# Optimization experiments

Hardware: AMD Instinct MI355X
Metric: run time of the kernel (lower is better)

The kernel has to match this reference:

```python
import jax, jax.numpy as jnp
import numpy as np

N, D = 1024, 512
BS, N_TEXT, N_VIDEO = 64, 16, 16
BETA = 1.0
N_ITERS = 50


def setup_inputs() -> dict:
    key = jax.random.key(0)
    k1, k2 = jax.random.split(key)
    return {
        "t_prob": jax.random.normal(k1, (N, D), dtype=jnp.float32),
        "v_prob": jax.random.normal(k2, (N, D), dtype=jnp.float32),
        "n": N,
        "bs": BS,
        "n_text": N_TEXT,
        "n_video": N_VIDEO,
    }


def _l2norm(x):
    # matches F.normalize(x, p=2, dim=1) (eps irrelevant for randn inputs)
    return x / jnp.linalg.norm(x, axis=1, keepdims=True)


def reference(t_prob, v_prob, n, bs, n_text, n_video):
    dt = t_prob.dtype
    x = _l2norm(t_prob)
    y = _l2norm(v_prob)
    C = 1.0 - x @ y.T                      # [n, n] cosine distance
    A = jnp.exp(-C / BETA)

    sigma0 = jnp.ones((n, 1), dtype=dt) / n
    T0 = jnp.ones((n, n), dtype=dt)

    def step(carry, _):
        T, sigma = carry
        Q = A * T                          # [n, n]
        delta = 1.0 / (n * (Q @ sigma))    # [n, 1]
        sigma_new = 1.0 / (n * (Q.T @ delta))  # [n, 1]
        # diag(delta) @ Q @ diag(sigma) == row/col rescale
        T_new = delta * Q * sigma_new.T
        return (T_new, sigma_new), None

    (T, _), _ = jax.lax.scan(step, (T0, sigma0), None, length=N_ITERS)

    distance_matrix = C.T @ T              # [n, n]
    distance_matrix = distance_matrix.reshape(bs, n_text, bs, n_video).mean(axis=(1, 3))
    dis_loss = jnp.trace(distance_matrix)
    return distance_matrix, dis_loss
```

## Files before the change

kernel.cpp:

```cpp
#include <hip/hip_runtime.h>
#include <math.h>


#define NWG 32
#define TPB 1024
#define NIT 50
#define NREP 4

typedef unsigned long long ull;

constexpr int CL_OFF   = 0;
constexpr int CVEC_OFF = 1024 * 1024;
constexpr int CNT_OFF  = CVEC_OFF + 3 * NREP * 1024;

__global__ __launch_bounds__(256) void k_gemm(const float* __restrict__ X,
                                              const float* __restrict__ Y,
                                              float* __restrict__ ws) {
    __shared__ float As[32][68];
    __shared__ float Bs[32][68];
    __shared__ float nX[64], nY[64];
    float* Cl = ws + CL_OFF;

    int tid = threadIdx.x;
    int tx = tid & 15, ty = tid >> 4;
    int bx = blockIdx.x, by = blockIdx.y;
    int lr0 = tid >> 3;
    int kq  = (tid & 7) * 4;

    float acc[4][4] = {};
    float sx0 = 0.f, sx1 = 0.f, sy0 = 0.f, sy1 = 0.f;
    for (int k0 = 0; k0 < 512; k0 += 32) {
        float4 xa = *(const float4*)(X + (size_t)(by * 64 + lr0) * 512 + k0 + kq);
        float4 xb = *(const float4*)(X + (size_t)(by * 64 + lr0 + 32) * 512 + k0 + kq);
        float4 ya = *(const float4*)(Y + (size_t)(bx * 64 + lr0) * 512 + k0 + kq);
        float4 yb = *(const float4*)(Y + (size_t)(bx * 64 + lr0 + 32) * 512 + k0 + kq);
        sx0 += xa.x * xa.x + xa.y * xa.y + xa.z * xa.z + xa.w * xa.w;
        sx1 += xb.x * xb.x + xb.y * xb.y + xb.z * xb.z + xb.w * xb.w;
        sy0 += ya.x * ya.x + ya.y * ya.y + ya.z * ya.z + ya.w * ya.w;
        sy1 += yb.x * yb.x + yb.y * yb.y + yb.z * yb.z + yb.w * yb.w;
        As[kq + 0][lr0] = xa.x; As[kq + 1][lr0] = xa.y;
        As[kq + 2][lr0] = xa.z; As[kq + 3][lr0] = xa.w;
        As[kq + 0][lr0 + 32] = xb.x; As[kq + 1][lr0 + 32] = xb.y;
        As[kq + 2][lr0 + 32] = xb.z; As[kq + 3][lr0 + 32] = xb.w;
        Bs[kq + 0][lr0] = ya.x; Bs[kq + 1][lr0] = ya.y;
        Bs[kq + 2][lr0] = ya.z; Bs[kq + 3][lr0] = ya.w;
        Bs[kq + 0][lr0 + 32] = yb.x; Bs[kq + 1][lr0 + 32] = yb.y;
        Bs[kq + 2][lr0 + 32] = yb.z; Bs[kq + 3][lr0 + 32] = yb.w;
        __syncthreads();
#pragma unroll
        for (int kk = 0; kk < 32; ++kk) {
            float4 a4 = *(const float4*)&As[kk][4 * ty];
            float4 b4 = *(const float4*)&Bs[kk][4 * tx];
            float av[4] = {a4.x, a4.y, a4.z, a4.w};
            float bv[4] = {b4.x, b4.y, b4.z, b4.w};
#pragma unroll
            for (int r = 0; r < 4; ++r)
#pragma unroll
                for (int q = 0; q < 4; ++q) acc[r][q] += av[r] * bv[q];
        }
        __syncthreads();
    }
#pragma unroll
    for (int m = 1; m < 8; m <<= 1) {
        sx0 += __shfl_xor(sx0, m, 64);
        sx1 += __shfl_xor(sx1, m, 64);
        sy0 += __shfl_xor(sy0, m, 64);
        sy1 += __shfl_xor(sy1, m, 64);
    }
    if ((tid & 7) == 0) {
        nX[lr0] = sx0; nX[lr0 + 32] = sx1;
        nY[lr0] = sy0; nY[lr0 + 32] = sy1;
    }
    __syncthreads();

    int i0 = by * 64 + 4 * ty, j0 = bx * 64 + 4 * tx;
    float vy[4];
#pragma unroll
    for (int q = 0; q < 4; ++q) vy[q] = 1.0f / sqrtf(nY[4 * tx + q]);
#pragma unroll
    for (int r = 0; r < 4; ++r) {
        float vx = 1.0f / sqrtf(nX[4 * ty + r]);
        float4 o;
        o.x = acc[r][0] * vx * vy[0] - 1.0f;
        o.y = acc[r][1] * vx * vy[1] - 1.0f;
        o.z = acc[r][2] * vx * vy[2] - 1.0f;
        o.w = acc[r][3] * vx * vy[3] - 1.0f;
        *(float4*)(Cl + (size_t)(i0 + r) * 1024 + j0) = o;
    }
}

__global__ __launch_bounds__(1024, 4) void k_ipot(float* __restrict__ ws,
                                                  float* __restrict__ out) {
    __shared__ float sL[1024];
    __shared__ float aL[32];
    __shared__ float buf[16 * 1024];
    __shared__ float twv[16];

    const int g = blockIdx.x, tid = threadIdx.x;
    const int rs = tid >> 6, lane = tid & 63;
    float* Cl   = ws + CL_OFF;
    float* cvec = ws + CVEC_OFF;
    unsigned* grp = (unsigned*)(ws + CNT_OFF);

    float C[2][16], E[2][16];
#pragma unroll
    for (int i = 0; i < 2; ++i) {
        const float* src = Cl + (size_t)(g * 32 + rs * 2 + i) * 1024 + lane * 16;
#pragma unroll
        for (int q = 0; q < 4; ++q) {
            float4 c = *(const float4*)(src + 4 * q);
            C[i][4 * q + 0] = c.x; C[i][4 * q + 1] = c.y;
            C[i][4 * q + 2] = c.z; C[i][4 * q + 3] = c.w;
        }
    }
#pragma unroll
    for (int i = 0; i < 2; ++i)
#pragma unroll
        for (int u = 0; u < 16; ++u) E[i][u] = __expf(C[i][u]);

    float bv = 1.0f;

    for (int t = 0; t < NIT; ++t) {
        if (t == 0) {
            sL[tid] = 1.0f / 1024.0f;
        } else {
            if (tid == 0) {
                unsigned tgt = (unsigned)t * 8u;
                long gd = 0;
                while (__hip_atomic_load(&grp[0], __ATOMIC_RELAXED, __HIP_MEMORY_SCOPE_AGENT) < tgt ||
                       __hip_atomic_load(&grp[1], __ATOMIC_RELAXED, __HIP_MEMORY_SCOPE_AGENT) < tgt ||
                       __hip_atomic_load(&grp[2], __ATOMIC_RELAXED, __HIP_MEMORY_SCOPE_AGENT) < tgt ||
                       __hip_atomic_load(&grp[3], __ATOMIC_RELAXED, __HIP_MEMORY_SCOPE_AGENT) < tgt) {
                    __builtin_amdgcn_s_sleep(1);
                    if (++gd > 2000000) break;
                }
            }
            __syncthreads();
            const float* rb = cvec + ((t + 2) % 3) * (NREP * 1024) + tid;
            float r0 = __hip_atomic_load(rb + 0 * 1024, __ATOMIC_RELAXED, __HIP_MEMORY_SCOPE_AGENT);
            float r1 = __hip_atomic_load(rb + 1 * 1024, __ATOMIC_RELAXED, __HIP_MEMORY_SCOPE_AGENT);
            float r2 = __hip_atomic_load(rb + 2 * 1024, __ATOMIC_RELAXED, __HIP_MEMORY_SCOPE_AGENT);
            float r3 = __hip_atomic_load(rb + 3 * 1024, __ATOMIC_RELAXED, __HIP_MEMORY_SCOPE_AGENT);
            if (t >= 2 && tid < 64) {
                ull* zb = (ull*)(cvec + ((t + 1) % 3) * (NREP * 1024)) + g * 64 + tid;
                __hip_atomic_store(zb, 0ull, __ATOMIC_RELAXED, __HIP_MEMORY_SCOPE_AGENT);
            }
            float c = r0 + r1 + r2 + r3;
            float b = 1.0f / c;
            sL[tid] = b * b / bv * (1.0f / 1024.0f);
            bv = b;
        }
        __syncthreads();

        float sv[16];
#pragma unroll
        for (int q = 0; q < 4; ++q) {
            float4 s4 = *(const float4*)&sL[lane * 16 + 4 * q];
            sv[4 * q + 0] = s4.x; sv[4 * q + 1] = s4.y;
            sv[4 * q + 2] = s4.z; sv[4 * q + 3] = s4.w;
        }
        float rp[2];
#pragma unroll
        for (int i = 0; i < 2; ++i) {
            float a = 0.0f;
#pragma unroll
            for (int u = 0; u < 16; ++u) a += E[i][u] * sv[u];
            rp[i] = a;
        }
#pragma unroll
        for (int m = 1; m < 64; m <<= 1) {
            rp[0] += __shfl_xor(rp[0], m, 64);
            rp[1] += __shfl_xor(rp[1], m, 64);
        }
        if (lane == 0) {
            aL[rs * 2 + 0] = 1.0f / (1024.0f * rp[0]);
            aL[rs * 2 + 1] = 1.0f / (1024.0f * rp[1]);
        }
        __syncthreads();

        float av0 = aL[rs * 2 + 0], av1 = aL[rs * 2 + 1];
#pragma unroll
        for (int q = 0; q < 4; ++q) {
            float4 o;
            o.x = E[0][4*q+0] * av0 + E[1][4*q+0] * av1;
            o.y = E[0][4*q+1] * av0 + E[1][4*q+1] * av1;
            o.z = E[0][4*q+2] * av0 + E[1][4*q+2] * av1;
            o.w = E[0][4*q+3] * av0 + E[1][4*q+3] * av1;
            *(float4*)&buf[rs * 1024 + lane * 16 + 4 * q] = o;
        }
        __syncthreads();

        float csum = 0.0f;
#pragma unroll
        for (int w = 0; w < 16; ++w) csum += buf[w * 1024 + tid];
        float* wb = cvec + (t % 3) * (NREP * 1024) + (g & 3) * 1024 + tid;
        atomicAdd(wb, csum);
        __syncthreads();
        if (tid == 0)
            __hip_atomic_fetch_add(&grp[g >> 3], 1u, __ATOMIC_RELAXED,
                                   __HIP_MEMORY_SCOPE_AGENT);

        if (t < NIT - 1) {
            const float kf = (float)(t + 2);
#pragma unroll
            for (int i = 0; i < 2; ++i)
#pragma unroll
                for (int u = 0; u < 16; ++u) E[i][u] = __expf(kf * C[i][u]);
        }
    }

    if (tid == 0) {
        unsigned tgt = (unsigned)NIT * 8u;
        long gd = 0;
        while (__hip_atomic_load(&grp[0], __ATOMIC_RELAXED, __HIP_MEMORY_SCOPE_AGENT) < tgt ||
               __hip_atomic_load(&grp[1], __ATOMIC_RELAXED, __HIP_MEMORY_SCOPE_AGENT) < tgt ||
               __hip_atomic_load(&grp[2], __ATOMIC_RELAXED, __HIP_MEMORY_SCOPE_AGENT) < tgt ||
               __hip_atomic_load(&grp[3], __ATOMIC_RELAXED, __HIP_MEMORY_SCOPE_AGENT) < tgt) {
            __builtin_amdgcn_s_sleep(1);
            if (++gd > 2000000) break;
        }
    }
    __syncthreads();
    {
        const float* rb = cvec + ((NIT - 1) % 3) * (NREP * 1024) + tid;
        float r0 = __hip_atomic_load(rb + 0 * 1024, __ATOMIC_RELAXED, __HIP_MEMORY_SCOPE_AGENT);
        float r1 = __hip_atomic_load(rb + 1 * 1024, __ATOMIC_RELAXED, __HIP_MEMORY_SCOPE_AGENT);
        float r2 = __hip_atomic_load(rb + 2 * 1024, __ATOMIC_RELAXED, __HIP_MEMORY_SCOPE_AGENT);
        float r3 = __hip_atomic_load(rb + 3 * 1024, __ATOMIC_RELAXED, __HIP_MEMORY_SCOPE_AGENT);
        sL[tid] = 1.0f / (r0 + r1 + r2 + r3);
    }
    __syncthreads();

    float* Ps = buf;
    float* Rs = buf + 2048;
    float bl[16];
#pragma unroll
    for (int q = 0; q < 4; ++q) {
        float4 b4 = *(const float4*)&sL[lane * 16 + 4 * q];
        bl[4 * q + 0] = b4.x; bl[4 * q + 1] = b4.y;
        bl[4 * q + 2] = b4.z; bl[4 * q + 3] = b4.w;
    }
#pragma unroll
    for (int i = 0; i < 2; ++i) {
        float p = 0.0f, r = 0.0f;
#pragma unroll
        for (int u = 0; u < 16; ++u) {
            p += C[i][u];
            r += E[i][u] * bl[u];
        }
        Ps[(rs * 2 + i) * 64 + lane] = -p;
        Rs[(rs * 2 + i) * 64 + lane] = aL[rs * 2 + i] * r;
    }
    __syncthreads();

    float Rk[32];
#pragma unroll
    for (int k = 0; k < 32; ++k) Rk[k] = Rs[k * 64 + lane];
    const float sc = 1.0f / (256.0f * 1024.0f);
    float tsum = 0.0f;
#pragma unroll
    for (int q = 0; q < 4; ++q) {
        int o = tid + 1024 * q;
        int A = o >> 6;
        float acc = 0.0f;
#pragma unroll
        for (int k = 0; k < 32; ++k) acc += Ps[k * 64 + A] * Rk[k];
        float val = acc * sc;
        atomicAdd(out + o, val);
        if (A == lane) tsum += val;
    }
#pragma unroll
    for (int m = 1; m < 64; m <<= 1) tsum += __shfl_xor(tsum, m, 64);
    if (lane == 0) twv[rs] = tsum;
    __syncthreads();
    if (tid == 0) {
        float ts = 0.0f;
#pragma unroll
        for (int w = 0; w < 16; ++w) ts += twv[w];
        atomicAdd(out + 4096, ts);
    }
}

extern "C" void kernel_launch(void* const* d_in, const int* in_sizes, int n_in,
                              void* d_out, int out_size, void* d_ws, size_t ws_size,
                              hipStream_t stream) {
    const float* X = (const float*)d_in[0];
    const float* Y = (const float*)d_in[1];
    float* out = (float*)d_out;
    float* ws  = (float*)d_ws;

    (void)hipMemsetAsync((char*)d_ws + (size_t)CVEC_OFF * 4, 0,
                         (3 * NREP * 1024 + 16) * 4, stream);
    (void)hipMemsetAsync(d_out, 0, (size_t)out_size * 4, stream);

    k_gemm<<<dim3(16, 16), 256, 0, stream>>>(X, Y, ws);
    k_ipot<<<NWG, TPB, 0, stream>>>(ws, out);
}
```

Measured before the change: 347.1 us.

## Replace counter-based grid barrier with sign-tagged per-block partial slots

Each block now stores its column partial sums into its own slot with a sign tag that alternates by iteration, instead of atomically adding into shared replicas and bumping group counters. Every thread polls all 32 slots directly until each tag shows the data is fresh, which removes the atomic adds, the counter barrier, the extra __syncthreads and the slot-zeroing stores. Shared memory is re-laid out with padding and a transposed ordering to avoid bank conflicts, and one block-level sync per iteration is dropped by computing the row scales in registers. In exchange each thread issues 32 polling loads per iteration, and correctness relies on the tagged values never being zero or carrying the wrong sign.

```diff
diff --git a/kernel.cpp b/kernel.cpp
--- a/kernel.cpp
+++ b/kernel.cpp
@@ -5,13 +5,11 @@
 #define NWG 32
 #define TPB 1024
 #define NIT 50
-#define NREP 4
 
 typedef unsigned long long ull;
 
 constexpr int CL_OFF   = 0;
 constexpr int CVEC_OFF = 1024 * 1024;
-constexpr int CNT_OFF  = CVEC_OFF + 3 * NREP * 1024;
 
 __global__ __launch_bounds__(256) void k_gemm(const float* __restrict__ X,
                                               const float* __restrict__ Y,
@@ -91,16 +89,15 @@
 
 __global__ __launch_bounds__(1024, 4) void k_ipot(float* __restrict__ ws,
                                                   float* __restrict__ out) {
-    __shared__ float sL[1024];
-    __shared__ float aL[32];
-    __shared__ float buf[16 * 1024];
+    __shared__ float sLp[1056];
+    __shared__ float buf[16 * 1056];
     __shared__ float twv[16];
 
     const int g = blockIdx.x, tid = threadIdx.x;
     const int rs = tid >> 6, lane = tid & 63;
+    const int uo = tid & 15, lo = tid >> 4;
     float* Cl   = ws + CL_OFF;
     float* cvec = ws + CVEC_OFF;
-    unsigned* grp = (unsigned*)(ws + CNT_OFF);
 
     float C[2][16], E[2][16];
 #pragma unroll
@@ -119,86 +116,69 @@
         for (int u = 0; u < 16; ++u) E[i][u] = __expf(C[i][u]);
 
     float bv = 1.0f;
+    float a0 = 0.0f, a1 = 0.0f;
 
     for (int t = 0; t < NIT; ++t) {
+        float sval;
         if (t == 0) {
-            sL[tid] = 1.0f / 1024.0f;
+            sval = 1.0f / 1024.0f;
         } else {
-            if (tid == 0) {
-                unsigned tgt = (unsigned)t * 8u;
-                long gd = 0;
-                while (__hip_atomic_load(&grp[0], __ATOMIC_RELAXED, __HIP_MEMORY_SCOPE_AGENT) < tgt ||
-                       __hip_atomic_load(&grp[1], __ATOMIC_RELAXED, __HIP_MEMORY_SCOPE_AGENT) < tgt ||
-                       __hip_atomic_load(&grp[2], __ATOMIC_RELAXED, __HIP_MEMORY_SCOPE_AGENT) < tgt ||
-                       __hip_atomic_load(&grp[3], __ATOMIC_RELAXED, __HIP_MEMORY_SCOPE_AGENT) < tgt) {
-                    __builtin_amdgcn_s_sleep(1);
-                    if (++gd > 2000000) break;
+            const float* rb = cvec + ((t - 1) % 3) * (NWG * 1024) + tid;
+            const bool expneg = ((t - 1) & 1) == 0;
+            float ssum = 0.0f;
+            long gd = 0;
+            for (;;) {
+                ssum = 0.0f;
+                unsigned bad = 0u;
+#pragma unroll
+                for (int s2 = 0; s2 < NWG; ++s2) {
+                    float v = __hip_atomic_load(rb + s2 * 1024, __ATOMIC_RELAXED,
+                                                __HIP_MEMORY_SCOPE_AGENT);
+                    unsigned bits = __float_as_uint(v);
+                    bad |= expneg ? (unsigned)(bits <= 0x80000000u)
+                                  : (unsigned)(bits == 0u || bits >= 0x80000000u);
+                    ssum += v;
                 }
+                if (!bad) break;
+                if (++gd > 100000) break;
+                __builtin_amdgcn_s_sleep(1);
             }
-            __syncthreads();
-            const float* rb = cvec + ((t + 2) % 3) * (NREP * 1024) + tid;
-            float r0 = __hip_atomic_load(rb + 0 * 1024, __ATOMIC_RELAXED, __HIP_MEMORY_SCOPE_AGENT);
-            float r1 = __hip_atomic_load(rb + 1 * 1024, __ATOMIC_RELAXED, __HIP_MEMORY_SCOPE_AGENT);
-            float r2 = __hip_atomic_load(rb + 2 * 1024, __ATOMIC_RELAXED, __HIP_MEMORY_SCOPE_AGENT);
-            float r3 = __hip_atomic_load(rb + 3 * 1024, __ATOMIC_RELAXED, __HIP_MEMORY_SCOPE_AGENT);
-            if (t >= 2 && tid < 64) {
-                ull* zb = (ull*)(cvec + ((t + 1) % 3) * (NREP * 1024)) + g * 64 + tid;
-                __hip_atomic_store(zb, 0ull, __ATOMIC_RELAXED, __HIP_MEMORY_SCOPE_AGENT);
-            }
-            float c = r0 + r1 + r2 + r3;
+            float c = expneg ? -ssum : ssum;
             float b = 1.0f / c;
-            sL[tid] = b * b / bv * (1.0f / 1024.0f);
+            sval = b * b / bv * (1.0f / 1024.0f);
             bv = b;
         }
+        sLp[uo * 66 + lo] = sval;
         __syncthreads();
 
         float sv[16];
 #pragma unroll
-        for (int q = 0; q < 4; ++q) {
-            float4 s4 = *(const float4*)&sL[lane * 16 + 4 * q];
-            sv[4 * q + 0] = s4.x; sv[4 * q + 1] = s4.y;
-            sv[4 * q + 2] = s4.z; sv[4 * q + 3] = s4.w;
-        }
-        float rp[2];
-#pragma unroll
-        for (int i = 0; i < 2; ++i) {
-            float a = 0.0f;
-#pragma unroll
-            for (int u = 0; u < 16; ++u) a += E[i][u] * sv[u];
-            rp[i] = a;
+        for (int u = 0; u < 16; ++u) sv[u] = sLp[u * 66 + lane];
+        float rp0 = 0.0f, rp1 = 0.0f;
+#pragma unroll
+        for (int u = 0; u < 16; ++u) {
+            rp0 += E[0][u] * sv[u];
+            rp1 += E[1][u] * sv[u];
         }
 #pragma unroll
         for (int m = 1; m < 64; m <<= 1) {
-            rp[0] += __shfl_xor(rp[0], m, 64);
-            rp[1] += __shfl_xor(rp[1], m, 64);
-        }
-        if (lane == 0) {
-            aL[rs * 2 + 0] = 1.0f / (1024.0f * rp[0]);
-            aL[rs * 2 + 1] = 1.0f / (1024.0f * rp[1]);
-        }
-        __syncthreads();
-
-        float av0 = aL[rs * 2 + 0], av1 = aL[rs * 2 + 1];
-#pragma unroll
-        for (int q = 0; q < 4; ++q) {
-            float4 o;
-            o.x = E[0][4*q+0] * av0 + E[1][4*q+0] * av1;
-            o.y = E[0][4*q+1] * av0 + E[1][4*q+1] * av1;
-            o.z = E[0][4*q+2] * av0 + E[1][4*q+2] * av1;
-            o.w = E[0][4*q+3] * av0 + E[1][4*q+3] * av1;
-            *(float4*)&buf[rs * 1024 + lane * 16 + 4 * q] = o;
-        }
+            rp0 += __shfl_xor(rp0, m, 64);
+            rp1 += __shfl_xor(rp1, m, 64);
+        }
+        a0 = 1.0f / (1024.0f * rp0);
+        a1 = 1.0f / (1024.0f * rp1);
+
+#pragma unroll
+        for (int u = 0; u < 16; ++u)
+            buf[rs * 1056 + u * 66 + lane] = E[0][u] * a0 + E[1][u] * a1;
         __syncthreads();
 
         float csum = 0.0f;
 #pragma unroll
-        for (int w = 0; w < 16; ++w) csum += buf[w * 1024 + tid];
-        float* wb = cvec + (t % 3) * (NREP * 1024) + (g & 3) * 1024 + tid;
-        atomicAdd(wb, csum);
-        __syncthreads();
-        if (tid == 0)
-            __hip_atomic_fetch_add(&grp[g >> 3], 1u, __ATOMIC_RELAXED,
-                                   __HIP_MEMORY_SCOPE_AGENT);
+        for (int w = 0; w < 16; ++w) csum += buf[w * 1056 + uo * 66 + lo];
+        float tagged = (t & 1) ? csum : -csum;
+        __hip_atomic_store(cvec + (t % 3) * (NWG * 1024) + g * 1024 + tid, tagged,
+                           __ATOMIC_RELAXED, __HIP_MEMORY_SCOPE_AGENT);
 
         if (t < NIT - 1) {
             const float kf = (float)(t + 2);
@@ -209,25 +189,26 @@
         }
     }
 
-    if (tid == 0) {
-        unsigned tgt = (unsigned)NIT * 8u;
+    {
+        const float* rb = cvec + ((NIT - 1) % 3) * (NWG * 1024) + tid;
+        float ssum = 0.0f;
         long gd = 0;
-        while (__hip_atomic_load(&grp[0], __ATOMIC_RELAXED, __HIP_MEMORY_SCOPE_AGENT) < tgt ||
-               __hip_atomic_load(&grp[1], __ATOMIC_RELAXED, __HIP_MEMORY_SCOPE_AGENT) < tgt ||
-               __hip_atomic_load(&grp[2], __ATOMIC_RELAXED, __HIP_MEMORY_SCOPE_AGENT) < tgt ||
-               __hip_atomic_load(&grp[3], __ATOMIC_RELAXED, __HIP_MEMORY_SCOPE_AGENT) < tgt) {
+        for (;;) {
+            ssum = 0.0f;
+            unsigned bad = 0u;
+#pragma unroll
+            for (int s2 = 0; s2 < NWG; ++s2) {
+                float v = __hip_atomic_load(rb + s2 * 1024, __ATOMIC_RELAXED,
+                                            __HIP_MEMORY_SCOPE_AGENT);
+                unsigned bits = __float_as_uint(v);
+                bad |= (unsigned)(bits == 0u || bits >= 0x80000000u);
+                ssum += v;
+            }
+            if (!bad) break;
+            if (++gd > 100000) break;
             __builtin_amdgcn_s_sleep(1);
-            if (++gd > 2000000) break;
-        }
-    }
-    __syncthreads();
-    {
-        const float* rb = cvec + ((NIT - 1) % 3) * (NREP * 1024) + tid;
-        float r0 = __hip_atomic_load(rb + 0 * 1024, __ATOMIC_RELAXED, __HIP_MEMORY_SCOPE_AGENT);
-        float r1 = __hip_atomic_load(rb + 1 * 1024, __ATOMIC_RELAXED, __HIP_MEMORY_SCOPE_AGENT);
-        float r2 = __hip_atomic_load(rb + 2 * 1024, __ATOMIC_RELAXED, __HIP_MEMORY_SCOPE_AGENT);
-        float r3 = __hip_atomic_load(rb + 3 * 1024, __ATOMIC_RELAXED, __HIP_MEMORY_SCOPE_AGENT);
-        sL[tid] = 1.0f / (r0 + r1 + r2 + r3);
+        }
+        sLp[uo * 66 + lo] = 1.0f / ssum;
     }
     __syncthreads();
 
@@ -235,21 +216,18 @@
     float* Rs = buf + 2048;
     float bl[16];
 #pragma unroll
-    for (int q = 0; q < 4; ++q) {
-        float4 b4 = *(const float4*)&sL[lane * 16 + 4 * q];
-        bl[4 * q + 0] = b4.x; bl[4 * q + 1] = b4.y;
-        bl[4 * q + 2] = b4.z; bl[4 * q + 3] = b4.w;
-    }
-#pragma unroll
-    for (int i = 0; i < 2; ++i) {
-        float p = 0.0f, r = 0.0f;
+    for (int u = 0; u < 16; ++u) bl[u] = sLp[u * 66 + lane];
+    {
+        float p0 = 0.0f, r0 = 0.0f, p1 = 0.0f, r1 = 0.0f;
 #pragma unroll
         for (int u = 0; u < 16; ++u) {
-            p += C[i][u];
-            r += E[i][u] * bl[u];
-        }
-        Ps[(rs * 2 + i) * 64 + lane] = -p;
-        Rs[(rs * 2 + i) * 64 + lane] = aL[rs * 2 + i] * r;
+            p0 += C[0][u]; r0 += E[0][u] * bl[u];
+            p1 += C[1][u]; r1 += E[1][u] * bl[u];
+        }
+        Ps[(rs * 2 + 0) * 64 + lane] = -p0;
+        Rs[(rs * 2 + 0) * 64 + lane] = a0 * r0;
+        Ps[(rs * 2 + 1) * 64 + lane] = -p1;
+        Rs[(rs * 2 + 1) * 64 + lane] = a1 * r1;
     }
     __syncthreads();
 
@@ -290,7 +268,7 @@
     float* ws  = (float*)d_ws;
 
     (void)hipMemsetAsync((char*)d_ws + (size_t)CVEC_OFF * 4, 0,
-                         (3 * NREP * 1024 + 16) * 4, stream);
+                         (size_t)(3 * NWG * 1024) * 4, stream);
     (void)hipMemsetAsync(d_out, 0, (size_t)out_size * 4, stream);
 
     k_gemm<<<dim3(16, 16), 256, 0, stream>>>(X, Y, ws);
```

Result: slower. 520.0 us (+49.8%).
